# Performance work log

Hardware: AMD Instinct MI355X
Metric: run time of the kernel (lower is better)

## Reference

```python
import jax, jax.numpy as jnp
import numpy as np

# irrep multiplicities from '128x0e + 64x1o + 32x2e' -> '64x0e + 16x2e' -> '1x0e + 1x2e'
N0E, N1O, N2E = 128, 64, 32   # node irreps multiplicities
H0E, H2E = 64, 16             # hidden irreps multiplicities
EPS = 1e-12                   # smooth-norm epsilon in Gate invariant


def silu(x):
    return x * jax.nn.sigmoid(x)


def setup_inputs() -> dict:
    key = jax.random.key(0)
    ks = jax.random.split(key, 16)
    N, G = 262144, 8192
    return {
        "node_scalar": jax.random.normal(ks[0], (N, 128), jnp.float32),
        "node_equi": jax.random.normal(ks[1], (N, 480), jnp.float32),
        "batch": jax.random.randint(ks[2], (N,), 0, G),
        # o3.Linear(node_irreps -> hidden_irreps), biases on 0e only
        "W_eq0": jax.random.normal(ks[3], (N0E, H0E), jnp.float32),
        "b_eq0": jnp.zeros((H0E,), jnp.float32),
        "W_eq2": jax.random.normal(ks[4], (N2E, H2E), jnp.float32),
        # o3.Linear(hidden_irreps -> 1x0e + 1x2e), bias on 0e only
        "W_out0": jax.random.normal(ks[5], (H0E, 1), jnp.float32),
        "b_out0": jnp.zeros((1,), jnp.float32),
        "W_out2": jax.random.normal(ks[6], (H2E,), jnp.float32),
        # scalar_out_mlp: Linear(128,64) -> silu -> Linear(64,2), biases init zero
        "Ws1": jax.random.normal(ks[7], (128, 64), jnp.float32) * 0.05,
        "bs1": jnp.zeros((64,), jnp.float32),
        "Ws2": jax.random.normal(ks[8], (64, 2), jnp.float32) * 0.05,
        "bs2": jnp.zeros((2,), jnp.float32),
        "n_graphs": G,
    }


def reference(node_scalar, node_equi, batch, W_eq0, b_eq0, W_eq2,
              W_out0, b_out0, W_out2, Ws1, bs1, Ws2, bs2, n_graphs):
    N = node_scalar.shape[0]
    # split e3nn-layout node features: [128x0e | 64x1o (192) | 32x2e (160)]
    x0 = node_equi[:, :N0E]                       # [N,128] scalars
    x2 = node_equi[:, N0E + 3 * N1O:].reshape(N, N2E, 5)  # [N,32,5] 2e block (1o dropped)

    # o3.Linear node->hidden (fan-in normalized), biases on scalars only
    h0 = x0 @ W_eq0 * (N0E ** -0.5) + b_eq0                       # [N,64]
    h2 = jnp.einsum('nmi,mk->nki', x2, W_eq2) * (N2E ** -0.5)     # [N,16,5]

    # Gate: x * act(per-irrep invariant norm)
    g0 = h0 * silu(jnp.sqrt(h0 * h0 + EPS))                       # [N,64]
    n2 = jnp.sqrt(jnp.sum(h2 * h2, axis=-1) + EPS)                # [N,16]
    g2 = h2 * silu(n2)[..., None]                                 # [N,16,5]

    # o3.Linear hidden -> 1x0e + 1x2e
    o0 = g0 @ W_out0 * (H0E ** -0.5) + b_out0                     # [N,1]
    o2 = jnp.einsum('nmi,m->ni', g2, W_out2) * (H2E ** -0.5)      # [N,5]

    # scalar MLP -> two gating scalars (2x0e)
    s = silu(node_scalar @ Ws1 + bs1) @ Ws2 + bs2                 # [N,2]

    # ElementwiseTensorProduct('1x0e + 1x2e', '2x0e')
    src = jnp.concatenate([o0 * s[:, :1], o2 * s[:, 1:2]], axis=-1)  # [N,6]

    # scatter_sum over graph index
    polar = jax.ops.segment_sum(src, batch, num_segments=n_graphs)   # [G,6]

    zero = polar[:, 0]
    dxy, dyz, dz2, dzx, dx2y2 = (polar[:, i] for i in range(1, 6))
    dn = jnp.sqrt(jnp.sum(polar[:, 1:6] ** 2, axis=-1))
    c = 3.0 ** -0.5
    xx = c * (dn - dz2) + dx2y2 + zero
    yy = c * (dn - dz2) - dx2y2 + zero
    zz = c * (dn + 2.0 * dz2) + zero
    row0 = jnp.stack([xx, dxy, dzx], axis=-1)
    row1 = jnp.stack([dxy, yy, dyz], axis=-1)
    row2 = jnp.stack([dzx, dyz, zz], axis=-1)
    return jnp.stack([row0, row1, row2], axis=-2)  # [G,3,3] polarizability
```

## Files before the change

### kernel.cpp

```cpp
#include <hip/hip_runtime.h>
#include <stdint.h>


__device__ __forceinline__ float fast_rcp(float x) {
    return __builtin_amdgcn_rcpf(x);
}

#define GEMM8(ACC, W, A0, A1)                                   \
    _Pragma("unroll")                                           \
    for (int j = 0; j < 64; j++) {                              \
        float v = (ACC)[j];                                     \
        v = fmaf((A0).x, (W)[j],       v);                      \
        v = fmaf((A0).y, (W)[64 + j],  v);                      \
        v = fmaf((A0).z, (W)[128 + j], v);                      \
        v = fmaf((A0).w, (W)[192 + j], v);                      \
        v = fmaf((A1).x, (W)[256 + j], v);                      \
        v = fmaf((A1).y, (W)[320 + j], v);                      \
        v = fmaf((A1).z, (W)[384 + j], v);                      \
        v = fmaf((A1).w, (W)[448 + j], v);                      \
        (ACC)[j] = v;                                           \
    }

__global__ __launch_bounds__(256, 4) void node_kernel(
    const float* __restrict__ node_scalar,
    const float* __restrict__ node_equi,
    const int*   __restrict__ batch,
    const float* __restrict__ Weq0,
    const float* __restrict__ beq0,
    const float* __restrict__ Weq2,
    const float* __restrict__ Wout0,
    const float* __restrict__ bout0,
    const float* __restrict__ Wout2,
    const float* __restrict__ Ws1,
    const float* __restrict__ bs1,
    const float* __restrict__ Ws2,
    const float* __restrict__ bs2,
    float* __restrict__ polar,
    int N)
{
    int n = blockIdx.x * 256 + threadIdx.x;
    if (n >= N) return;
    int b = batch[n];

    float acc[64];

#pragma unroll
    for (int j = 0; j < 64; j++) acc[j] = 0.f;
    const float4* nsr = (const float4*)(node_scalar + (size_t)n * 128);
    {
        float4 a0 = nsr[0], a1 = nsr[1];
#pragma unroll 1
        for (int c = 0; c < 15; c++) {
            float4 b0 = nsr[2 * c + 2], b1 = nsr[2 * c + 3];
            const float* w = Ws1 + c * 512;
            GEMM8(acc, w, a0, a1);
            a0 = b0; a1 = b1;
        }
        GEMM8(acc, Ws1 + 15 * 512, a0, a1);
    }
    float sA = bs2[0], sB = bs2[1];
#pragma unroll
    for (int j = 0; j < 64; j++) {
        float h = acc[j] + bs1[j];
        float t = h * fast_rcp(1.f + __expf(-h));
        sA = fmaf(t, Ws2[2 * j],     sA);
        sB = fmaf(t, Ws2[2 * j + 1], sB);
    }

#pragma unroll
    for (int j = 0; j < 64; j++) acc[j] = 0.f;
    const float4* x0r = (const float4*)(node_equi + (size_t)n * 480);
    {
        float4 a0 = x0r[0], a1 = x0r[1];
#pragma unroll 1
        for (int c = 0; c < 15; c++) {
            float4 b0 = x0r[2 * c + 2], b1 = x0r[2 * c + 3];
            const float* w = Weq0 + c * 512;
            GEMM8(acc, w, a0, a1);
            a0 = b0; a1 = b1;
        }
        GEMM8(acc, Weq0 + 15 * 512, a0, a1);
    }
    float o0 = 0.f;
#pragma unroll
    for (int j = 0; j < 64; j++) {
        float h = fmaf(acc[j], 0.08838834764831845f, beq0[j]);
        float r = sqrtf(fmaf(h, h, 1e-12f));
        float g = h * (r * fast_rcp(1.f + __expf(-r)));
        o0 = fmaf(g, Wout0[j], o0);
    }
    o0 = fmaf(o0, 0.125f, bout0[0]);

    const float4* x2r = (const float4*)(node_equi + (size_t)n * 480 + 320);
    float o2[5] = { 0.f, 0.f, 0.f, 0.f, 0.f };
    const float S32 = 0.17677669529663687f;
#pragma unroll 1
    for (int kc = 0; kc < 2; kc++) {
        float acc2h[40];
#pragma unroll
        for (int t = 0; t < 40; t++) acc2h[t] = 0.f;
        float4 c0 = x2r[0], c1 = x2r[1], c2 = x2r[2], c3 = x2r[3], c4 = x2r[4];
#pragma unroll 1
        for (int mc = 0; mc < 8; mc++) {
            float4 n0, n1, n2, n3, n4;
            if (mc < 7) {
                n0 = x2r[mc * 5 + 5]; n1 = x2r[mc * 5 + 6];
                n2 = x2r[mc * 5 + 7]; n3 = x2r[mc * 5 + 8];
                n4 = x2r[mc * 5 + 9];
            }
            float f[20] = { c0.x, c0.y, c0.z, c0.w, c1.x,
                            c1.y, c1.z, c1.w, c2.x, c2.y,
                            c2.z, c2.w, c3.x, c3.y, c3.z,
                            c3.w, c4.x, c4.y, c4.z, c4.w };
#pragma unroll
            for (int mm = 0; mm < 4; mm++) {
                float v0 = f[mm * 5 + 0], v1 = f[mm * 5 + 1],
                      v2 = f[mm * 5 + 2], v3 = f[mm * 5 + 3],
                      v4 = f[mm * 5 + 4];
                const float* wq = Weq2 + (mc * 4 + mm) * 16 + kc * 8;
#pragma unroll
                for (int kk = 0; kk < 8; kk++) {
                    float wk = wq[kk];
                    acc2h[kk * 5 + 0] = fmaf(v0, wk, acc2h[kk * 5 + 0]);
                    acc2h[kk * 5 + 1] = fmaf(v1, wk, acc2h[kk * 5 + 1]);
                    acc2h[kk * 5 + 2] = fmaf(v2, wk, acc2h[kk * 5 + 2]);
                    acc2h[kk * 5 + 3] = fmaf(v3, wk, acc2h[kk * 5 + 3]);
                    acc2h[kk * 5 + 4] = fmaf(v4, wk, acc2h[kk * 5 + 4]);
                }
            }
            c0 = n0; c1 = n1; c2 = n2; c3 = n3; c4 = n4;
        }
#pragma unroll
        for (int kk = 0; kk < 8; kk++) {
            float h0 = acc2h[kk * 5 + 0] * S32, h1 = acc2h[kk * 5 + 1] * S32,
                  h2 = acc2h[kk * 5 + 2] * S32, h3 = acc2h[kk * 5 + 3] * S32,
                  h4 = acc2h[kk * 5 + 4] * S32;
            float nn = sqrtf(h0 * h0 + h1 * h1 + h2 * h2 + h3 * h3 +
                             h4 * h4 + 1e-12f);
            float sil = nn * fast_rcp(1.f + __expf(-nn));
            float fct = sil * Wout2[kc * 8 + kk];
            o2[0] = fmaf(h0, fct, o2[0]); o2[1] = fmaf(h1, fct, o2[1]);
            o2[2] = fmaf(h2, fct, o2[2]); o2[3] = fmaf(h3, fct, o2[3]);
            o2[4] = fmaf(h4, fct, o2[4]);
        }
    }

    float* p = polar + (size_t)b * 6;
    atomicAdd(p + 0, o0 * sA);
    float q = 0.25f * sB;
    atomicAdd(p + 1, o2[0] * q);
    atomicAdd(p + 2, o2[1] * q);
    atomicAdd(p + 3, o2[2] * q);
    atomicAdd(p + 4, o2[3] * q);
    atomicAdd(p + 5, o2[4] * q);
}

__global__ __launch_bounds__(256) void finalize_kernel(
    const float* __restrict__ polar, float* __restrict__ out, int G)
{
    int g = blockIdx.x * 256 + threadIdx.x;
    if (g >= G) return;
    const float* p = polar + (size_t)g * 6;
    float z = p[0], dxy = p[1], dyz = p[2], dz2 = p[3], dzx = p[4], dx2 = p[5];
    float dn = sqrtf(dxy * dxy + dyz * dyz + dz2 * dz2 + dzx * dzx + dx2 * dx2);
    const float c = 0.57735026918962576f;
    float xx = c * (dn - dz2) + dx2 + z;
    float yy = c * (dn - dz2) - dx2 + z;
    float zz = c * (dn + 2.f * dz2) + z;
    float* o = out + (size_t)g * 9;
    o[0] = xx;  o[1] = dxy; o[2] = dzx;
    o[3] = dxy; o[4] = yy;  o[5] = dyz;
    o[6] = dzx; o[7] = dyz; o[8] = zz;
}

extern "C" void kernel_launch(void* const* d_in, const int* in_sizes, int n_in,
                              void* d_out, int out_size, void* d_ws, size_t ws_size,
                              hipStream_t stream) {
    const float* node_scalar = (const float*)d_in[0];
    const float* node_equi   = (const float*)d_in[1];
    const int*   batch       = (const int*)d_in[2];
    const float* Weq0  = (const float*)d_in[3];
    const float* beq0  = (const float*)d_in[4];
    const float* Weq2  = (const float*)d_in[5];
    const float* Wout0 = (const float*)d_in[6];
    const float* bout0 = (const float*)d_in[7];
    const float* Wout2 = (const float*)d_in[8];
    const float* Ws1   = (const float*)d_in[9];
    const float* bs1   = (const float*)d_in[10];
    const float* Ws2   = (const float*)d_in[11];
    const float* bs2   = (const float*)d_in[12];

    int N = in_sizes[0] / 128;
    int G = out_size / 9;
    float* polar = (float*)d_ws;

    hipMemsetAsync(polar, 0, (size_t)G * 6 * sizeof(float), stream);

    node_kernel<<<(N + 255) / 256, 256, 0, stream>>>(
        node_scalar, node_equi, batch,
        Weq0, beq0, Weq2, Wout0, bout0, Wout2, Ws1, bs1, Ws2, bs2,
        polar, N);

    finalize_kernel<<<(G + 255) / 256, 256, 0, stream>>>(
        polar, (float*)d_out, G);
}
```

Baseline: 1.061 ms.

## Split each node's hidden outputs across four waves with LDS reduction

Each node is now handled by four wavefronts, each computing a 16-wide slice of the 64 hidden units (and 4 of the 16 l=2 channels), instead of one thread computing all 64. Partial sums are combined through shared memory, and one wave performs the atomic scatter. This cuts per-thread register pressure (acc from 64 to 16 floats) so more waves can be resident, and splits the weight work across threads. In exchange, each node's input rows are loaded four times (served by cache), and the kernel adds a block barrier plus shared-memory traffic.

```diff
diff --git a/kernel.cpp b/kernel.cpp
--- a/kernel.cpp
+++ b/kernel.cpp
@@ -6,9 +6,9 @@
     return __builtin_amdgcn_rcpf(x);
 }
 
-#define GEMM8(ACC, W, A0, A1)                                   \
+#define GEMM8x16(ACC, W, A0, A1)                                \
     _Pragma("unroll")                                           \
-    for (int j = 0; j < 64; j++) {                              \
+    for (int j = 0; j < 16; j++) {                              \
         float v = (ACC)[j];                                     \
         v = fmaf((A0).x, (W)[j],       v);                      \
         v = fmaf((A0).y, (W)[64 + j],  v);                      \
@@ -21,7 +21,7 @@
         (ACC)[j] = v;                                           \
     }
 
-__global__ __launch_bounds__(256, 4) void node_kernel(
+__global__ __launch_bounds__(256) void node_kernel(
     const float* __restrict__ node_scalar,
     const float* __restrict__ node_equi,
     const int*   __restrict__ batch,
@@ -38,121 +38,137 @@
     float* __restrict__ polar,
     int N)
 {
-    int n = blockIdx.x * 256 + threadIdx.x;
-    if (n >= N) return;
-    int b = batch[n];
-
-    float acc[64];
-
-#pragma unroll
-    for (int j = 0; j < 64; j++) acc[j] = 0.f;
-    const float4* nsr = (const float4*)(node_scalar + (size_t)n * 128);
+    const int lane = threadIdx.x & 63;
+    const int s    = threadIdx.x >> 6;
+    const int n    = blockIdx.x * 64 + lane;
+    const bool valid = (n < N);
+    const int n_ld = valid ? n : (N - 1);
+
+    float acc[16];
+#pragma unroll
+    for (int j = 0; j < 16; j++) acc[j] = 0.f;
+    const float4* nsr = (const float4*)(node_scalar + (size_t)n_ld * 128);
     {
         float4 a0 = nsr[0], a1 = nsr[1];
 #pragma unroll 1
         for (int c = 0; c < 15; c++) {
             float4 b0 = nsr[2 * c + 2], b1 = nsr[2 * c + 3];
-            const float* w = Ws1 + c * 512;
-            GEMM8(acc, w, a0, a1);
+            const float* w = Ws1 + c * 512 + s * 16;
+            GEMM8x16(acc, w, a0, a1);
             a0 = b0; a1 = b1;
         }
-        GEMM8(acc, Ws1 + 15 * 512, a0, a1);
-    }
-    float sA = bs2[0], sB = bs2[1];
-#pragma unroll
-    for (int j = 0; j < 64; j++) {
-        float h = acc[j] + bs1[j];
+        GEMM8x16(acc, Ws1 + 15 * 512 + s * 16, a0, a1);
+    }
+    float sAp = 0.f, sBp = 0.f;
+#pragma unroll
+    for (int j = 0; j < 16; j++) {
+        int jg = s * 16 + j;
+        float h = acc[j] + bs1[jg];
         float t = h * fast_rcp(1.f + __expf(-h));
-        sA = fmaf(t, Ws2[2 * j],     sA);
-        sB = fmaf(t, Ws2[2 * j + 1], sB);
-    }
-
-#pragma unroll
-    for (int j = 0; j < 64; j++) acc[j] = 0.f;
-    const float4* x0r = (const float4*)(node_equi + (size_t)n * 480);
+        sAp = fmaf(t, Ws2[2 * jg],     sAp);
+        sBp = fmaf(t, Ws2[2 * jg + 1], sBp);
+    }
+
+#pragma unroll
+    for (int j = 0; j < 16; j++) acc[j] = 0.f;
+    const float4* x0r = (const float4*)(node_equi + (size_t)n_ld * 480);
     {
         float4 a0 = x0r[0], a1 = x0r[1];
 #pragma unroll 1
         for (int c = 0; c < 15; c++) {
             float4 b0 = x0r[2 * c + 2], b1 = x0r[2 * c + 3];
-            const float* w = Weq0 + c * 512;
-            GEMM8(acc, w, a0, a1);
+            const float* w = Weq0 + c * 512 + s * 16;
+            GEMM8x16(acc, w, a0, a1);
             a0 = b0; a1 = b1;
         }
-        GEMM8(acc, Weq0 + 15 * 512, a0, a1);
-    }
-    float o0 = 0.f;
-#pragma unroll
-    for (int j = 0; j < 64; j++) {
-        float h = fmaf(acc[j], 0.08838834764831845f, beq0[j]);
+        GEMM8x16(acc, Weq0 + 15 * 512 + s * 16, a0, a1);
+    }
+    float o0p = 0.f;
+#pragma unroll
+    for (int j = 0; j < 16; j++) {
+        int jg = s * 16 + j;
+        float h = fmaf(acc[j], 0.08838834764831845f, beq0[jg]);
         float r = sqrtf(fmaf(h, h, 1e-12f));
         float g = h * (r * fast_rcp(1.f + __expf(-r)));
-        o0 = fmaf(g, Wout0[j], o0);
-    }
-    o0 = fmaf(o0, 0.125f, bout0[0]);
-
-    const float4* x2r = (const float4*)(node_equi + (size_t)n * 480 + 320);
-    float o2[5] = { 0.f, 0.f, 0.f, 0.f, 0.f };
+        o0p = fmaf(g, Wout0[jg], o0p);
+    }
+
+    float acc2[20];
+#pragma unroll
+    for (int t = 0; t < 20; t++) acc2[t] = 0.f;
+    const float4* x2r = (const float4*)(node_equi + (size_t)n_ld * 480 + 320);
+#pragma unroll 1
+    for (int mc = 0; mc < 8; mc++) {
+        float4 c0 = x2r[mc * 5 + 0], c1 = x2r[mc * 5 + 1],
+               c2 = x2r[mc * 5 + 2], c3 = x2r[mc * 5 + 3],
+               c4 = x2r[mc * 5 + 4];
+        float f[20] = { c0.x, c0.y, c0.z, c0.w, c1.x,
+                        c1.y, c1.z, c1.w, c2.x, c2.y,
+                        c2.z, c2.w, c3.x, c3.y, c3.z,
+                        c3.w, c4.x, c4.y, c4.z, c4.w };
+#pragma unroll
+        for (int mm = 0; mm < 4; mm++) {
+            float v0 = f[mm * 5 + 0], v1 = f[mm * 5 + 1],
+                  v2 = f[mm * 5 + 2], v3 = f[mm * 5 + 3],
+                  v4 = f[mm * 5 + 4];
+            const float* wq = Weq2 + (mc * 4 + mm) * 16 + s * 4;
+#pragma unroll
+            for (int kk = 0; kk < 4; kk++) {
+                float wk = wq[kk];
+                acc2[kk * 5 + 0] = fmaf(v0, wk, acc2[kk * 5 + 0]);
+                acc2[kk * 5 + 1] = fmaf(v1, wk, acc2[kk * 5 + 1]);
+                acc2[kk * 5 + 2] = fmaf(v2, wk, acc2[kk * 5 + 2]);
+                acc2[kk * 5 + 3] = fmaf(v3, wk, acc2[kk * 5 + 3]);
+                acc2[kk * 5 + 4] = fmaf(v4, wk, acc2[kk * 5 + 4]);
+            }
+        }
+    }
+    float o2p[5] = { 0.f, 0.f, 0.f, 0.f, 0.f };
     const float S32 = 0.17677669529663687f;
-#pragma unroll 1
-    for (int kc = 0; kc < 2; kc++) {
-        float acc2h[40];
-#pragma unroll
-        for (int t = 0; t < 40; t++) acc2h[t] = 0.f;
-        float4 c0 = x2r[0], c1 = x2r[1], c2 = x2r[2], c3 = x2r[3], c4 = x2r[4];
-#pragma unroll 1
-        for (int mc = 0; mc < 8; mc++) {
-            float4 n0, n1, n2, n3, n4;
-            if (mc < 7) {
-                n0 = x2r[mc * 5 + 5]; n1 = x2r[mc * 5 + 6];
-                n2 = x2r[mc * 5 + 7]; n3 = x2r[mc * 5 + 8];
-                n4 = x2r[mc * 5 + 9];
-            }
-            float f[20] = { c0.x, c0.y, c0.z, c0.w, c1.x,
-                            c1.y, c1.z, c1.w, c2.x, c2.y,
-                            c2.z, c2.w, c3.x, c3.y, c3.z,
-                            c3.w, c4.x, c4.y, c4.z, c4.w };
-#pragma unroll
-            for (int mm = 0; mm < 4; mm++) {
-                float v0 = f[mm * 5 + 0], v1 = f[mm * 5 + 1],
-                      v2 = f[mm * 5 + 2], v3 = f[mm * 5 + 3],
-                      v4 = f[mm * 5 + 4];
-                const float* wq = Weq2 + (mc * 4 + mm) * 16 + kc * 8;
-#pragma unroll
-                for (int kk = 0; kk < 8; kk++) {
-                    float wk = wq[kk];
-                    acc2h[kk * 5 + 0] = fmaf(v0, wk, acc2h[kk * 5 + 0]);
-                    acc2h[kk * 5 + 1] = fmaf(v1, wk, acc2h[kk * 5 + 1]);
-                    acc2h[kk * 5 + 2] = fmaf(v2, wk, acc2h[kk * 5 + 2]);
-                    acc2h[kk * 5 + 3] = fmaf(v3, wk, acc2h[kk * 5 + 3]);
-                    acc2h[kk * 5 + 4] = fmaf(v4, wk, acc2h[kk * 5 + 4]);
-                }
-            }
-            c0 = n0; c1 = n1; c2 = n2; c3 = n3; c4 = n4;
-        }
-#pragma unroll
-        for (int kk = 0; kk < 8; kk++) {
-            float h0 = acc2h[kk * 5 + 0] * S32, h1 = acc2h[kk * 5 + 1] * S32,
-                  h2 = acc2h[kk * 5 + 2] * S32, h3 = acc2h[kk * 5 + 3] * S32,
-                  h4 = acc2h[kk * 5 + 4] * S32;
-            float nn = sqrtf(h0 * h0 + h1 * h1 + h2 * h2 + h3 * h3 +
-                             h4 * h4 + 1e-12f);
-            float sil = nn * fast_rcp(1.f + __expf(-nn));
-            float fct = sil * Wout2[kc * 8 + kk];
-            o2[0] = fmaf(h0, fct, o2[0]); o2[1] = fmaf(h1, fct, o2[1]);
-            o2[2] = fmaf(h2, fct, o2[2]); o2[3] = fmaf(h3, fct, o2[3]);
-            o2[4] = fmaf(h4, fct, o2[4]);
-        }
-    }
-
-    float* p = polar + (size_t)b * 6;
-    atomicAdd(p + 0, o0 * sA);
-    float q = 0.25f * sB;
-    atomicAdd(p + 1, o2[0] * q);
-    atomicAdd(p + 2, o2[1] * q);
-    atomicAdd(p + 3, o2[2] * q);
-    atomicAdd(p + 4, o2[3] * q);
-    atomicAdd(p + 5, o2[4] * q);
+#pragma unroll
+    for (int kk = 0; kk < 4; kk++) {
+        float h0 = acc2[kk * 5 + 0] * S32, h1 = acc2[kk * 5 + 1] * S32,
+              h2 = acc2[kk * 5 + 2] * S32, h3 = acc2[kk * 5 + 3] * S32,
+              h4 = acc2[kk * 5 + 4] * S32;
+        float nn = sqrtf(h0 * h0 + h1 * h1 + h2 * h2 + h3 * h3 +
+                         h4 * h4 + 1e-12f);
+        float sil = nn * fast_rcp(1.f + __expf(-nn));
+        float fct = sil * Wout2[s * 4 + kk];
+        o2p[0] = fmaf(h0, fct, o2p[0]); o2p[1] = fmaf(h1, fct, o2p[1]);
+        o2p[2] = fmaf(h2, fct, o2p[2]); o2p[3] = fmaf(h3, fct, o2p[3]);
+        o2p[4] = fmaf(h4, fct, o2p[4]);
+    }
+
+    __shared__ float red[4][64][9];
+    {
+        float* r = &red[s][lane][0];
+        r[0] = sAp; r[1] = sBp; r[2] = o0p;
+        r[3] = o2p[0]; r[4] = o2p[1]; r[5] = o2p[2];
+        r[6] = o2p[3]; r[7] = o2p[4];
+    }
+    __syncthreads();
+    if (s == 0 && valid) {
+        float vA = 0.f, vB = 0.f, v0 = 0.f,
+              w0 = 0.f, w1 = 0.f, w2 = 0.f, w3 = 0.f, w4 = 0.f;
+#pragma unroll
+        for (int w = 0; w < 4; w++) {
+            const float* q = &red[w][lane][0];
+            vA += q[0]; vB += q[1]; v0 += q[2];
+            w0 += q[3]; w1 += q[4]; w2 += q[5]; w3 += q[6]; w4 += q[7];
+        }
+        float sA = vA + bs2[0];
+        float sB = vB + bs2[1];
+        float o0 = fmaf(v0, 0.125f, bout0[0]);
+        int b = batch[n];
+        float* p = polar + (size_t)b * 6;
+        atomicAdd(p + 0, o0 * sA);
+        float q2 = 0.25f * sB;
+        atomicAdd(p + 1, w0 * q2);
+        atomicAdd(p + 2, w1 * q2);
+        atomicAdd(p + 3, w2 * q2);
+        atomicAdd(p + 4, w3 * q2);
+        atomicAdd(p + 5, w4 * q2);
+    }
 }
 
 __global__ __launch_bounds__(256) void finalize_kernel(
@@ -196,7 +212,7 @@
 
     hipMemsetAsync(polar, 0, (size_t)G * 6 * sizeof(float), stream);
 
-    node_kernel<<<(N + 255) / 256, 256, 0, stream>>>(
+    node_kernel<<<(N + 63) / 64, 256, 0, stream>>>(
         node_scalar, node_equi, batch,
         Weq0, beq0, Weq2, Wout0, bout0, Wout2, Ws1, bs1, Ws2, bs2,
         polar, N);
```

New measurement: 1.395 ms. +31.6%, slower.
